# Performance work log

Hardware: AMD Instinct MI355X
Metric: run time of the kernel (lower is better)

Reference implementation:

```python
import jax, jax.numpy as jnp
import numpy as np

N_NODES = 2_000_000
N_FEAT = 64
N_GRAPHS = 4096


def setup_inputs() -> dict:
    key = jax.random.key(0)
    k1, k2 = jax.random.split(key)
    x = jax.random.normal(k1, (N_NODES, N_FEAT), dtype=jnp.float32)
    b = jnp.sort(jax.random.randint(k2, (N_NODES,), 0, N_GRAPHS, dtype=jnp.int64))
    return {"x": x, "b": b, "n_graphs": N_GRAPHS}


def reference(x, b, n_graphs):
    # Per-graph mean of feature column 0: single-pass segment mean.
    col = x[:, 0]                                            # [N]
    sums = jax.ops.segment_sum(col, b, num_segments=n_graphs)            # [G]
    counts = jax.ops.segment_sum(jnp.ones_like(col), b, num_segments=n_graphs)
    out = (sums / counts)[:, None]                           # [G, 1]
    return out
```

## Files before the change

### kernel.cpp

```cpp
#include <hip/hip_runtime.h>


__global__ void seg_mean_kernel(const float* __restrict__ x,
                                const int* __restrict__ b,
                                float* __restrict__ out,
                                int n, int nfeat) {
    int g = blockIdx.x;
    __shared__ int s_lb, s_ub;
    __shared__ float s_part[4];

    if (threadIdx.x == 0) {
        int lo = 0, hi = n;
        while (lo < hi) { int m = (lo + hi) >> 1; if (b[m] < g) lo = m + 1; else hi = m; }
        s_lb = lo;
    }
    if (threadIdx.x == 64) {
        int lo = 0, hi = n;
        while (lo < hi) { int m = (lo + hi) >> 1; if (b[m] <= g) lo = m + 1; else hi = m; }
        s_ub = lo;
    }
    __syncthreads();
    int lb = s_lb, ub = s_ub;

    float acc = 0.f;
    for (int i = lb + (int)threadIdx.x; i < ub; i += (int)blockDim.x)
        acc += x[(size_t)i * (size_t)nfeat];

    #pragma unroll
    for (int off = 32; off > 0; off >>= 1)
        acc += __shfl_down(acc, off, 64);
    if ((threadIdx.x & 63) == 0) s_part[threadIdx.x >> 6] = acc;
    __syncthreads();

    if (threadIdx.x == 0) {
        float s = s_part[0] + s_part[1] + s_part[2] + s_part[3];
        out[g] = s / (float)(ub - lb);
    }
}

extern "C" void kernel_launch(void* const* d_in, const int* in_sizes, int n_in,
                              void* d_out, int out_size, void* d_ws, size_t ws_size,
                              hipStream_t stream) {
    const float* x = (const float*)d_in[0];
    const int*   b = (const int*)d_in[1];
    int n     = in_sizes[1];
    int nfeat = in_sizes[0] / n;
    int ng    = out_size;

    seg_mean_kernel<<<ng, 256, 0, stream>>>(x, b, (float*)d_out, n, nfeat);
}
```

Measured before the change: 47.46 us.

## Use wave-wide 64-ary search for segment bounds and unroll nontemporal gather

Replaces the single-thread binary searches for segment bounds with a 64-way wave-parallel search using ballot, cutting the dependent global-load chain from about 21 steps to about 4. The accumulation loop is unrolled by two and uses nontemporal loads for the strided column-0 gather. The search issues 64 loads per step instead of one, and nontemporal hints may change cache behaviour.

New measurement: 46.06 us. 3.0% less time.

```diff
diff --git a/kernel.cpp b/kernel.cpp
--- a/kernel.cpp
+++ b/kernel.cpp
@@ -1,35 +1,60 @@
 #include <hip/hip_runtime.h>
 
 
-__global__ void seg_mean_kernel(const float* __restrict__ x,
-                                const int* __restrict__ b,
-                                float* __restrict__ out,
-                                int n, int nfeat) {
+__device__ __forceinline__ int lower_bound_wide(const int* __restrict__ b, int n,
+                                                int target, int lane) {
+    int lo = 0, hi = n;
+    while (hi > lo) {
+        long long span = (long long)(hi - lo);
+        int q = lo + (int)((span * lane) >> 6);
+        int v = b[q];
+        unsigned long long m = __ballot(v < target);
+        if (m == 0ULL) return lo;
+        int k = 63 - __clzll(m);
+        int qk  = lo + (int)((span * (long long)k) >> 6);
+        int qk1 = (k < 63) ? (lo + (int)((span * (long long)(k + 1)) >> 6)) : hi;
+        lo = qk + 1;
+        hi = qk1;
+    }
+    return lo;
+}
+
+__global__ __launch_bounds__(256)
+void seg_mean_kernel(const float* __restrict__ x,
+                     const int* __restrict__ b,
+                     float* __restrict__ out,
+                     int n, int nfeat) {
     int g = blockIdx.x;
+    int lane = threadIdx.x & 63;
+    int wave = threadIdx.x >> 6;
     __shared__ int s_lb, s_ub;
     __shared__ float s_part[4];
 
-    if (threadIdx.x == 0) {
-        int lo = 0, hi = n;
-        while (lo < hi) { int m = (lo + hi) >> 1; if (b[m] < g) lo = m + 1; else hi = m; }
-        s_lb = lo;
-    }
-    if (threadIdx.x == 64) {
-        int lo = 0, hi = n;
-        while (lo < hi) { int m = (lo + hi) >> 1; if (b[m] <= g) lo = m + 1; else hi = m; }
-        s_ub = lo;
+    if (wave == 0) {
+        int r = lower_bound_wide(b, n, g, lane);
+        if (lane == 0) s_lb = r;
+    } else if (wave == 1) {
+        int r = lower_bound_wide(b, n, g + 1, lane);
+        if (lane == 0) s_ub = r;
     }
     __syncthreads();
     int lb = s_lb, ub = s_ub;
 
     float acc = 0.f;
-    for (int i = lb + (int)threadIdx.x; i < ub; i += (int)blockDim.x)
-        acc += x[(size_t)i * (size_t)nfeat];
+    int i0 = lb + (int)threadIdx.x;
+    int stride = (int)blockDim.x;
+    for (; i0 + stride < ub; i0 += 2 * stride) {
+        float v0 = __builtin_nontemporal_load(x + (size_t)i0 * (size_t)nfeat);
+        float v1 = __builtin_nontemporal_load(x + (size_t)(i0 + stride) * (size_t)nfeat);
+        acc += v0 + v1;
+    }
+    if (i0 < ub)
+        acc += __builtin_nontemporal_load(x + (size_t)i0 * (size_t)nfeat);
 
     #pragma unroll
     for (int off = 32; off > 0; off >>= 1)
         acc += __shfl_down(acc, off, 64);
-    if ((threadIdx.x & 63) == 0) s_part[threadIdx.x >> 6] = acc;
+    if (lane == 0) s_part[wave] = acc;
     __syncthreads();
 
     if (threadIdx.x == 0) {
```
